# Performance work log

Hardware: AMD Instinct MI355X
Metric: run time of the kernel (lower is better)

The kernel has to match this reference:

```python
import jax, jax.numpy as jnp
from jax import lax
import numpy as np

K_NUM = 4
KD = KH = KW = 3
IN_CH = 32
OUT_CH = 64
ATT_HID = 8  # max(in_ch // max(4, min(8, in_ch//64)), 4) = max(32//4, 4)


def _build_freq_masks(kd, kh, kw, kernel_num):
    # Static (numpy) replica of build_3d_freq_masks: quantile-banded FFT energy masks.
    fd = np.fft.fftfreq(kd)
    fh = np.fft.fftfreq(kh)
    fw = np.fft.fftfreq(kw)
    FZ, FY, FX = np.meshgrid(fd, fh, fw, indexing='ij')
    energy = (FZ ** 2 + FY ** 2 + FX ** 2).ravel()
    bounds = np.quantile(energy, np.linspace(0.0, 1.0, kernel_num + 1), method='linear')
    masks = np.stack([(energy >= bounds[i]) & (energy <= bounds[i + 1]) for i in range(kernel_num)])
    return jnp.asarray(masks.reshape(kernel_num, kd, kh, kw), dtype=jnp.float32)


def setup_inputs() -> dict:
    key = jax.random.key(0)
    ks = jax.random.split(key, 7)
    x = jax.random.normal(ks[0], (2, IN_CH, 64, 64, 64), dtype=jnp.float32)
    freq_param = jax.random.normal(ks[1], (OUT_CH, IN_CH, KD, KH, KW, 2), dtype=jnp.float32) * 0.001
    att_w1 = jax.random.normal(ks[2], (ATT_HID, IN_CH), dtype=jnp.float32) * 0.1
    att_b1 = jnp.zeros((ATT_HID,), dtype=jnp.float32)
    att_w2 = jax.random.normal(ks[3], (K_NUM, ATT_HID), dtype=jnp.float32) * 0.1
    att_b2 = jnp.zeros((K_NUM,), dtype=jnp.float32)
    bias = jnp.zeros((OUT_CH,), dtype=jnp.float32)
    return {"x": x, "freq_param": freq_param, "att_w1": att_w1, "att_b1": att_b1,
            "att_w2": att_w2, "att_b2": att_b2, "bias": bias}


def reference(x, freq_param, att_w1, att_b1, att_w2, att_b2, bias):
    masks = _build_freq_masks(KD, KH, KW, K_NUM)  # (K, kd, kh, kw)
    # Frequency params -> complex -> banded -> spatial kernels via batched IFFT.
    freq = lax.complex(freq_param[..., 0], freq_param[..., 1])  # (O,I,kd,kh,kw) complex64
    masked = freq[None] * masks[:, None, None].astype(freq.dtype)  # (K,O,I,kd,kh,kw)
    kernels = jnp.fft.ifftn(masked, axes=(-3, -2, -1)).real.astype(x.dtype)
    # Per-sample attention over K experts: GAP -> 1x1 conv (linear) -> relu -> linear -> softmax.
    pooled = jnp.mean(x, axis=(2, 3, 4))  # (B, C)
    h = jax.nn.relu(pooled @ att_w1.T + att_b1)  # (B, hid)
    att = jax.nn.softmax(h @ att_w2.T + att_b2, axis=1)  # (B, K)
    out = jnp.zeros((x.shape[0], OUT_CH) + x.shape[2:], dtype=x.dtype)
    for k in range(K_NUM):  # fixed small expert count
        y_k = lax.conv_general_dilated(
            x, kernels[k], window_strides=(1, 1, 1),
            padding=[(1, 1)] * 3, rhs_dilation=(1, 1, 1),
            dimension_numbers=('NCDHW', 'OIDHW', 'NCDHW'))
        out = out + att[:, k][:, None, None, None, None] * y_k
    return out + bias[None, :, None, None, None]
```

## Files before the change

kernel.cpp:

```cpp
#include <hip/hip_runtime.h>

#define DIM 64
#define ICH 32
#define OCH 64
#define SPA (DIM*DIM*DIM)

typedef short  s16x8  __attribute__((ext_vector_type(8)));
typedef float  f32x16 __attribute__((ext_vector_type(16)));

__device__ __forceinline__ short f2bf(float f) {
    unsigned u = __float_as_uint(f);
    return (short)((u + 0x7fffu + ((u >> 16) & 1u)) >> 16);
}
__device__ __forceinline__ int swz(int a) { return a ^ (((a >> 7) & 7) << 4); }

__global__ __launch_bounds__(256) void pool_kernel(const float* __restrict__ x,
                                                   float* __restrict__ partial) {
    int bid = blockIdx.x;
    int pair = bid >> 5;
    int chunk = bid & 31;
    const float4* base = (const float4*)(x + (size_t)pair * SPA + (size_t)chunk * 8192);
    int tid = threadIdx.x;
    float s = 0.f;
#pragma unroll
    for (int k = 0; k < 8; ++k) {
        float4 v = base[k * 256 + tid];
        s += (v.x + v.y) + (v.z + v.w);
    }
#pragma unroll
    for (int off = 32; off > 0; off >>= 1) s += __shfl_down(s, off, 64);
    __shared__ float red[4];
    int lane = tid & 63, wv = tid >> 6;
    if (lane == 0) red[wv] = s;
    __syncthreads();
    if (tid == 0) partial[bid] = (red[0] + red[1]) + (red[2] + red[3]);
}

__global__ __launch_bounds__(64) void attn_kernel(const float* __restrict__ partial,
                                                  const float* __restrict__ w1,
                                                  const float* __restrict__ b1,
                                                  const float* __restrict__ w2,
                                                  const float* __restrict__ b2,
                                                  float* __restrict__ weff) {
    __shared__ float pl[64], hh[16], at[8];
    int t = threadIdx.x;
    {
        float s = 0.f;
#pragma unroll
        for (int k = 0; k < 32; ++k) s += partial[t * 32 + k];
        pl[t] = s * (1.0f / (float)SPA);
    }
    __syncthreads();
    if (t < 16) {
        int b = t >> 3, j = t & 7;
        float a = b1[j];
        for (int c = 0; c < 32; ++c) a += pl[b * 32 + c] * w1[j * 32 + c];
        hh[t] = a > 0.f ? a : 0.f;
    }
    __syncthreads();
    if (t < 8) {
        int b = t >> 2, k = t & 3;
        float a = b2[k];
        for (int j = 0; j < 8; ++j) a += hh[b * 8 + j] * w2[k * 8 + j];
        at[t] = a;
    }
    __syncthreads();
    if (t < 2) {
        float l0 = at[t*4], l1 = at[t*4+1], l2 = at[t*4+2], l3 = at[t*4+3];
        float m = fmaxf(fmaxf(l0, l1), fmaxf(l2, l3));
        float e0 = expf(l0 - m), e1 = expf(l1 - m), e2 = expf(l2 - m), e3 = expf(l3 - m);
        float inv = 1.0f / (e0 + e1 + e2 + e3);
        at[t*4] = e0 * inv; at[t*4+1] = e1 * inv; at[t*4+2] = e2 * inv; at[t*4+3] = e3 * inv;
    }
    __syncthreads();
    if (t < 54) {
        int b = t / 27, m = t % 27;
        int z = m / 9, y = (m / 3) % 3, xx = m % 3;
        int n = (z > 0) + (y > 0) + (xx > 0);
        float w = 0.f;
        w += at[b*4 + 0] * ((n <= 1) ? 1.f : 0.f);
        w += at[b*4 + 1] * ((n == 2) ? 1.f : 0.f);
        w += at[b*4 + 2] * ((n >= 2) ? 1.f : 0.f);
        w += at[b*4 + 3] * ((n == 3) ? 1.f : 0.f);
        weff[t] = w;
    }
}

__global__ __launch_bounds__(256) void ifft_kernel(const float* __restrict__ freq,
                                                   const float* __restrict__ weff,
                                                   short* __restrict__ keff) {
    int idx = blockIdx.x * 256 + threadIdx.x;
    int i = idx & 31;
    int o = (idx >> 5) & 63;
    int bt = idx >> 11;
    int t = bt % 27, b = bt / 27;
    int d = t / 9, h = (t / 3) % 3, w = t % 3;
    const float* f = freq + (size_t)(o * 32 + i) * 54;
    float s = 0.f;
#pragma unroll
    for (int z = 0; z < 3; ++z)
#pragma unroll
        for (int y = 0; y < 3; ++y)
#pragma unroll
            for (int xk = 0; xk < 3; ++xk) {
                int m = (d * z + h * y + w * xk) % 3;
                float cm = (m == 0) ? 1.0f : -0.5f;
                float sm = (m == 0) ? 0.0f : ((m == 1) ? 0.8660254037844386f
                                                       : -0.8660254037844386f);
                int tap = z * 9 + y * 3 + xk;
                s += weff[b * 27 + tap] * (f[tap * 2] * cm - f[tap * 2 + 1] * sm);
            }
    keff[idx] = f2bf(s * (1.0f / 27.0f));
}

__global__ __launch_bounds__(256, 2) void conv_mfma(const float* __restrict__ x,
                                                    const short* __restrict__ keff,
                                                    const float* __restrict__ bias,
                                                    float* __restrict__ out) {
    __shared__ char xs[34560];

    int bid = blockIdx.x;
    int wblk = bid & 3;
    int hblk = (bid >> 2) & 7;
    int dblk = (bid >> 5) & 15;
    int b    = bid >> 9;
    int d0 = dblk * 4, h0 = hblk * 8, w0 = wblk * 16;

    int tid = threadIdx.x;
    int l = tid & 63, td = tid >> 6;

    f32x16 acc[2][4];
#pragma unroll
    for (int i = 0; i < 2; ++i)
#pragma unroll
        for (int j = 0; j < 4; ++j) acc[i][j] = f32x16{};

    int laneB = td * 5760 + ((l >> 4) & 1) * 576 + (l & 15) * 32 + (l >> 5) * 16;
    const short* Abase = keff + (size_t)b * 55296 + (l & 31) * 32 + (l >> 5) * 8;
    int p0 = tid >> 1, half = tid & 1;

    for (int chunk = 0; chunk < 2; ++chunk) {
        __syncthreads();
        const float* xc = x + (size_t)(b * ICH + chunk * 16 + half * 8) * SPA;
#pragma unroll
        for (int it = 0; it < 9; ++it) {
            int e = it * 256 + tid;
            if (e < 2160) {
                int p = it * 128 + p0;
                int dd = p / 180, r = p - dd * 180;
                int hh2 = r / 18, ww2 = r - hh2 * 18;
                int gd = d0 - 1 + dd, gh = h0 - 1 + hh2, gw = w0 - 1 + ww2;
                s16x8 v = {};
                if ((unsigned)gd < 64u && (unsigned)gh < 64u && (unsigned)gw < 64u) {
                    const float* xp = xc + (((gd * 64) + gh) * 64 + gw);
#pragma unroll
                    for (int j = 0; j < 8; ++j) v[j] = f2bf(xp[(size_t)j * SPA]);
                }
                *(s16x8*)(xs + swz(e * 16)) = v;
            }
        }
        __syncthreads();

        const short* A = Abase + chunk * 16;
        s16x8 a0 = *(const s16x8*)(A);
        s16x8 a1 = *(const s16x8*)(A + 1024);
#pragma unroll 1
        for (int tap = 0; tap < 27; ++tap) {
            int nxt = (tap < 26) ? tap + 1 : 26;
            s16x8 n0 = *(const s16x8*)(A + nxt * 2048);
            s16x8 n1 = *(const s16x8*)(A + nxt * 2048 + 1024);
            int kd = tap / 9, rr = tap - kd * 9;
            int kh = rr / 3, kw2 = rr - kh * 3;
            int off = laneB + kd * 5760 + kh * 576 + kw2 * 32;
            s16x8 B0 = *(const s16x8*)(xs + swz(off));
            s16x8 B1 = *(const s16x8*)(xs + swz(off + 1152));
            s16x8 B2 = *(const s16x8*)(xs + swz(off + 2304));
            s16x8 B3 = *(const s16x8*)(xs + swz(off + 3456));
            acc[0][0] = __builtin_amdgcn_mfma_f32_32x32x16_bf16(a0, B0, acc[0][0], 0, 0, 0);
            acc[1][0] = __builtin_amdgcn_mfma_f32_32x32x16_bf16(a1, B0, acc[1][0], 0, 0, 0);
            acc[0][1] = __builtin_amdgcn_mfma_f32_32x32x16_bf16(a0, B1, acc[0][1], 0, 0, 0);
            acc[1][1] = __builtin_amdgcn_mfma_f32_32x32x16_bf16(a1, B1, acc[1][1], 0, 0, 0);
            acc[0][2] = __builtin_amdgcn_mfma_f32_32x32x16_bf16(a0, B2, acc[0][2], 0, 0, 0);
            acc[1][2] = __builtin_amdgcn_mfma_f32_32x32x16_bf16(a1, B2, acc[1][2], 0, 0, 0);
            acc[0][3] = __builtin_amdgcn_mfma_f32_32x32x16_bf16(a0, B3, acc[0][3], 0, 0, 0);
            acc[1][3] = __builtin_amdgcn_mfma_f32_32x32x16_bf16(a1, B3, acc[1][3], 0, 0, 0);
            a0 = n0; a1 = n1;
        }
    }

    float bv[32];
#pragma unroll
    for (int ot = 0; ot < 2; ++ot)
#pragma unroll
        for (int reg = 0; reg < 16; ++reg)
            bv[ot * 16 + reg] = bias[ot * 32 + (reg & 3) + 8 * (reg >> 2) + 4 * (l >> 5)];

    int dd = d0 + td;
    int ww2 = w0 + (l & 15);
    int hbase = h0 + ((l >> 4) & 1);
#pragma unroll
    for (int ot = 0; ot < 2; ++ot)
#pragma unroll
        for (int s = 0; s < 4; ++s) {
#pragma unroll
            for (int reg = 0; reg < 16; ++reg) {
                int o = ot * 32 + (reg & 3) + 8 * (reg >> 2) + 4 * (l >> 5);
                size_t oidx = (((size_t)(b * OCH + o) * DIM + dd) * DIM
                               + (hbase + 2 * s)) * DIM + ww2;
                out[oidx] = acc[ot][s][reg] + bv[ot * 16 + reg];
            }
        }
}

extern "C" void kernel_launch(void* const* d_in, const int* in_sizes, int n_in,
                              void* d_out, int out_size, void* d_ws, size_t ws_size,
                              hipStream_t stream) {
    const float* x    = (const float*)d_in[0];
    const float* freq = (const float*)d_in[1];
    const float* w1   = (const float*)d_in[2];
    const float* b1   = (const float*)d_in[3];
    const float* w2   = (const float*)d_in[4];
    const float* b2   = (const float*)d_in[5];
    const float* bias = (const float*)d_in[6];
    float* out = (float*)d_out;
    float* ws  = (float*)d_ws;

    float* partial = ws;
    float* weff    = ws + 2048;
    short* keff    = (short*)(ws + 2048 + 64);

    pool_kernel<<<2048, 256, 0, stream>>>(x, partial);
    attn_kernel<<<1, 64, 0, stream>>>(partial, w1, b1, w2, b2, weff);
    ifft_kernel<<<432, 256, 0, stream>>>(freq, weff, keff);
    conv_mfma<<<1024, 256, 0, stream>>>(x, keff, bias, out);
}
```

Baseline: 279.9 us.

## Pre-transpose input to channel-last bf16 and fuse pooling, attention and IFFT

Adds a prepass kernel that computes pooling partial sums and, in the same pass, writes x as a channel-last bf16 tensor. The conv kernel can then load 16-byte contiguous channel vectors instead of eight strided fp32 loads with per-element conversion. Attention and kernel synthesis are merged into one kernel, with each block redundantly recomputing the attention weights, which removes a launch. The cost is an extra 32MB bf16 write and read plus a dependence on workspace size, with the old path kept as a fallback.

```diff
diff --git a/kernel.cpp b/kernel.cpp
--- a/kernel.cpp
+++ b/kernel.cpp
@@ -12,49 +12,86 @@
     unsigned u = __float_as_uint(f);
     return (short)((u + 0x7fffu + ((u >> 16) & 1u)) >> 16);
 }
+__device__ __forceinline__ unsigned pk2bf(float lo, float hi) {
+    return (unsigned)(unsigned short)f2bf(lo) | ((unsigned)(unsigned short)f2bf(hi) << 16);
+}
 __device__ __forceinline__ int swz(int a) { return a ^ (((a >> 7) & 7) << 4); }
 
-__global__ __launch_bounds__(256) void pool_kernel(const float* __restrict__ x,
-                                                   float* __restrict__ partial) {
+
+__global__ __launch_bounds__(256) void prepass_kernel(const float* __restrict__ x,
+                                                      short* __restrict__ xT,
+                                                      float* __restrict__ partial) {
+    __shared__ unsigned lds32[64 * 17];
+    __shared__ float pacc[32];
+
     int bid = blockIdx.x;
-    int pair = bid >> 5;
-    int chunk = bid & 31;
-    const float4* base = (const float4*)(x + (size_t)pair * SPA + (size_t)chunk * 8192);
-    int tid = threadIdx.x;
-    float s = 0.f;
-#pragma unroll
-    for (int k = 0; k < 8; ++k) {
-        float4 v = base[k * 256 + tid];
-        s += (v.x + v.y) + (v.z + v.w);
-    }
-#pragma unroll
-    for (int off = 32; off > 0; off >>= 1) s += __shfl_down(s, off, 64);
-    __shared__ float red[4];
-    int lane = tid & 63, wv = tid >> 6;
-    if (lane == 0) red[wv] = s;
-    __syncthreads();
-    if (tid == 0) partial[bid] = (red[0] + red[1]) + (red[2] + red[3]);
-}
-
-__global__ __launch_bounds__(64) void attn_kernel(const float* __restrict__ partial,
-                                                  const float* __restrict__ w1,
-                                                  const float* __restrict__ b1,
-                                                  const float* __restrict__ w2,
-                                                  const float* __restrict__ b2,
-                                                  float* __restrict__ weff) {
-    __shared__ float pl[64], hh[16], at[8];
+    int hq = bid & 15, d = (bid >> 4) & 63, b = bid >> 10;
+    int t = threadIdx.x;
+    int cp = t >> 4;
+    int wg = t & 15;
+
+    float acc0 = 0.f, acc1 = 0.f;
+
+    for (int r = 0; r < 4; ++r) {
+        int h = hq * 4 + r;
+        const float* s0 = x + (size_t)(b * ICH + 2 * cp) * SPA + (d * 4096 + h * 64 + wg * 4);
+        float4 a = *(const float4*)s0;
+        float4 c = *(const float4*)(s0 + SPA);
+        acc0 += (a.x + a.y) + (a.z + a.w);
+        acc1 += (c.x + c.y) + (c.z + c.w);
+        __syncthreads();
+        lds32[(wg * 4 + 0) * 17 + cp] = pk2bf(a.x, c.x);
+        lds32[(wg * 4 + 1) * 17 + cp] = pk2bf(a.y, c.y);
+        lds32[(wg * 4 + 2) * 17 + cp] = pk2bf(a.z, c.z);
+        lds32[(wg * 4 + 3) * 17 + cp] = pk2bf(a.w, c.w);
+        __syncthreads();
+        int w = t >> 2, q = t & 3;
+        uint4 v;
+        v.x = lds32[w * 17 + q * 4 + 0];
+        v.y = lds32[w * 17 + q * 4 + 1];
+        v.z = lds32[w * 17 + q * 4 + 2];
+        v.w = lds32[w * 17 + q * 4 + 3];
+        *(uint4*)(xT + ((size_t)((b * 64 + d) * 64 + h) * 64 + w) * 32 + q * 8) = v;
+    }
+#pragma unroll
+    for (int off = 1; off < 16; off <<= 1) {
+        acc0 += __shfl_down(acc0, off, 64);
+        acc1 += __shfl_down(acc1, off, 64);
+    }
+    if (wg == 0) { pacc[2 * cp] = acc0; pacc[2 * cp + 1] = acc1; }
+    __syncthreads();
+    if (t < 32) partial[(size_t)(b * 32 + t) * 1024 + d * 16 + hq] = pacc[t];
+}
+
+__global__ __launch_bounds__(256) void attn_ifft_kernel(const float* __restrict__ partial,
+                                                        const float* __restrict__ freq,
+                                                        const float* __restrict__ w1,
+                                                        const float* __restrict__ b1,
+                                                        const float* __restrict__ w2,
+                                                        const float* __restrict__ b2,
+                                                        short* __restrict__ keff) {
+    __shared__ float red[256];
+    __shared__ float pooled[64];
+    __shared__ float hh[16], at[8], we[54];
     int t = threadIdx.x;
     {
+        int p = t >> 2, q = t & 3;
+        const float4* src = (const float4*)(partial + (size_t)p * 1024 + q * 256);
         float s = 0.f;
 #pragma unroll
-        for (int k = 0; k < 32; ++k) s += partial[t * 32 + k];
-        pl[t] = s * (1.0f / (float)SPA);
-    }
+        for (int k = 0; k < 64; ++k) {
+            float4 v = src[k];
+            s += (v.x + v.y) + (v.z + v.w);
+        }
+        red[t] = s;
+    }
+    __syncthreads();
+    if (t < 64) pooled[t] = (red[4*t] + red[4*t+1] + red[4*t+2] + red[4*t+3]) * (1.0f / (float)SPA);
     __syncthreads();
     if (t < 16) {
         int b = t >> 3, j = t & 7;
         float a = b1[j];
-        for (int c = 0; c < 32; ++c) a += pl[b * 32 + c] * w1[j * 32 + c];
+        for (int c = 0; c < 32; ++c) a += pooled[b * 32 + c] * w1[j * 32 + c];
         hh[t] = a > 0.f ? a : 0.f;
     }
     __syncthreads();
@@ -82,19 +119,15 @@
         w += at[b*4 + 1] * ((n == 2) ? 1.f : 0.f);
         w += at[b*4 + 2] * ((n >= 2) ? 1.f : 0.f);
         w += at[b*4 + 3] * ((n == 3) ? 1.f : 0.f);
-        weff[t] = w;
-    }
-}
-
-__global__ __launch_bounds__(256) void ifft_kernel(const float* __restrict__ freq,
-                                                   const float* __restrict__ weff,
-                                                   short* __restrict__ keff) {
-    int idx = blockIdx.x * 256 + threadIdx.x;
+        we[t] = w;
+    }
+    __syncthreads();
+    int idx = blockIdx.x * 256 + t;
     int i = idx & 31;
     int o = (idx >> 5) & 63;
     int bt = idx >> 11;
-    int t = bt % 27, b = bt / 27;
-    int d = t / 9, h = (t / 3) % 3, w = t % 3;
+    int tp = bt % 27, b = bt / 27;
+    int dk = tp / 9, hk = (tp / 3) % 3, wk = tp % 3;
     const float* f = freq + (size_t)(o * 32 + i) * 54;
     float s = 0.f;
 #pragma unroll
@@ -103,17 +136,17 @@
         for (int y = 0; y < 3; ++y)
 #pragma unroll
             for (int xk = 0; xk < 3; ++xk) {
-                int m = (d * z + h * y + w * xk) % 3;
+                int m = (dk * z + hk * y + wk * xk) % 3;
                 float cm = (m == 0) ? 1.0f : -0.5f;
                 float sm = (m == 0) ? 0.0f : ((m == 1) ? 0.8660254037844386f
                                                        : -0.8660254037844386f);
                 int tap = z * 9 + y * 3 + xk;
-                s += weff[b * 27 + tap] * (f[tap * 2] * cm - f[tap * 2 + 1] * sm);
+                s += we[b * 27 + tap] * (f[tap * 2] * cm - f[tap * 2 + 1] * sm);
             }
     keff[idx] = f2bf(s * (1.0f / 27.0f));
 }
 
-__global__ __launch_bounds__(256, 2) void conv_mfma(const float* __restrict__ x,
+__global__ __launch_bounds__(256, 2) void conv_fast(const short* __restrict__ xT,
                                                     const short* __restrict__ keff,
                                                     const float* __restrict__ bias,
                                                     float* __restrict__ out) {
@@ -137,25 +170,22 @@
 
     int laneB = td * 5760 + ((l >> 4) & 1) * 576 + (l & 15) * 32 + (l >> 5) * 16;
     const short* Abase = keff + (size_t)b * 55296 + (l & 31) * 32 + (l >> 5) * 8;
-    int p0 = tid >> 1, half = tid & 1;
+    const short* xTb = xT + (size_t)b * 8388608;
 
     for (int chunk = 0; chunk < 2; ++chunk) {
         __syncthreads();
-        const float* xc = x + (size_t)(b * ICH + chunk * 16 + half * 8) * SPA;
-#pragma unroll
-        for (int it = 0; it < 9; ++it) {
+        const short* xc = xTb + chunk * 16;
+#pragma unroll
+        for (int it = 0; it < 17; ++it) {
             int e = it * 256 + tid;
-            if (e < 2160) {
-                int p = it * 128 + p0;
+            if (e < 4320) {
+                int p = e >> 1, hf = e & 1;
                 int dd = p / 180, r = p - dd * 180;
                 int hh2 = r / 18, ww2 = r - hh2 * 18;
                 int gd = d0 - 1 + dd, gh = h0 - 1 + hh2, gw = w0 - 1 + ww2;
                 s16x8 v = {};
-                if ((unsigned)gd < 64u && (unsigned)gh < 64u && (unsigned)gw < 64u) {
-                    const float* xp = xc + (((gd * 64) + gh) * 64 + gw);
-#pragma unroll
-                    for (int j = 0; j < 8; ++j) v[j] = f2bf(xp[(size_t)j * SPA]);
-                }
+                if ((unsigned)gd < 64u && (unsigned)gh < 64u && (unsigned)gw < 64u)
+                    v = *(const s16x8*)(xc + ((gd * 64 + gh) * 64 + gw) * 32 + hf * 8);
                 *(s16x8*)(xs + swz(e * 16)) = v;
             }
         }
@@ -212,6 +242,197 @@
         }
 }
 
+
+__global__ __launch_bounds__(256) void pool_kernel(const float* __restrict__ x,
+                                                   float* __restrict__ partial) {
+    int bid = blockIdx.x;
+    int pair = bid >> 5;
+    int chunk = bid & 31;
+    const float4* base = (const float4*)(x + (size_t)pair * SPA + (size_t)chunk * 8192);
+    int tid = threadIdx.x;
+    float s = 0.f;
+#pragma unroll
+    for (int k = 0; k < 8; ++k) {
+        float4 v = base[k * 256 + tid];
+        s += (v.x + v.y) + (v.z + v.w);
+    }
+#pragma unroll
+    for (int off = 32; off > 0; off >>= 1) s += __shfl_down(s, off, 64);
+    __shared__ float red[4];
+    int lane = tid & 63, wv = tid >> 6;
+    if (lane == 0) red[wv] = s;
+    __syncthreads();
+    if (tid == 0) partial[bid] = (red[0] + red[1]) + (red[2] + red[3]);
+}
+
+__global__ __launch_bounds__(64) void attn_kernel(const float* __restrict__ partial,
+                                                  const float* __restrict__ w1,
+                                                  const float* __restrict__ b1,
+                                                  const float* __restrict__ w2,
+                                                  const float* __restrict__ b2,
+                                                  float* __restrict__ weff) {
+    __shared__ float pl[64], hh[16], at[8];
+    int t = threadIdx.x;
+    {
+        float s = 0.f;
+#pragma unroll
+        for (int k = 0; k < 32; ++k) s += partial[t * 32 + k];
+        pl[t] = s * (1.0f / (float)SPA);
+    }
+    __syncthreads();
+    if (t < 16) {
+        int b = t >> 3, j = t & 7;
+        float a = b1[j];
+        for (int c = 0; c < 32; ++c) a += pl[b * 32 + c] * w1[j * 32 + c];
+        hh[t] = a > 0.f ? a : 0.f;
+    }
+    __syncthreads();
+    if (t < 8) {
+        int b = t >> 2, k = t & 3;
+        float a = b2[k];
+        for (int j = 0; j < 8; ++j) a += hh[b * 8 + j] * w2[k * 8 + j];
+        at[t] = a;
+    }
+    __syncthreads();
+    if (t < 2) {
+        float l0 = at[t*4], l1 = at[t*4+1], l2 = at[t*4+2], l3 = at[t*4+3];
+        float m = fmaxf(fmaxf(l0, l1), fmaxf(l2, l3));
+        float e0 = expf(l0 - m), e1 = expf(l1 - m), e2 = expf(l2 - m), e3 = expf(l3 - m);
+        float inv = 1.0f / (e0 + e1 + e2 + e3);
+        at[t*4] = e0 * inv; at[t*4+1] = e1 * inv; at[t*4+2] = e2 * inv; at[t*4+3] = e3 * inv;
+    }
+    __syncthreads();
+    if (t < 54) {
+        int b = t / 27, m = t % 27;
+        int z = m / 9, y = (m / 3) % 3, xx = m % 3;
+        int n = (z > 0) + (y > 0) + (xx > 0);
+        float w = 0.f;
+        w += at[b*4 + 0] * ((n <= 1) ? 1.f : 0.f);
+        w += at[b*4 + 1] * ((n == 2) ? 1.f : 0.f);
+        w += at[b*4 + 2] * ((n >= 2) ? 1.f : 0.f);
+        w += at[b*4 + 3] * ((n == 3) ? 1.f : 0.f);
+        weff[t] = w;
+    }
+}
+
+__global__ __launch_bounds__(256) void ifft_kernel(const float* __restrict__ freq,
+                                                   const float* __restrict__ weff,
+                                                   short* __restrict__ keff) {
+    int idx = blockIdx.x * 256 + threadIdx.x;
+    int i = idx & 31;
+    int o = (idx >> 5) & 63;
+    int bt = idx >> 11;
+    int t = bt % 27, b = bt / 27;
+    int d = t / 9, h = (t / 3) % 3, w = t % 3;
+    const float* f = freq + (size_t)(o * 32 + i) * 54;
+    float s = 0.f;
+#pragma unroll
+    for (int z = 0; z < 3; ++z)
+#pragma unroll
+        for (int y = 0; y < 3; ++y)
+#pragma unroll
+            for (int xk = 0; xk < 3; ++xk) {
+                int m = (d * z + h * y + w * xk) % 3;
+                float cm = (m == 0) ? 1.0f : -0.5f;
+                float sm = (m == 0) ? 0.0f : ((m == 1) ? 0.8660254037844386f
+                                                       : -0.8660254037844386f);
+                int tap = z * 9 + y * 3 + xk;
+                s += weff[b * 27 + tap] * (f[tap * 2] * cm - f[tap * 2 + 1] * sm);
+            }
+    keff[idx] = f2bf(s * (1.0f / 27.0f));
+}
+
+__global__ __launch_bounds__(256, 2) void conv_mfma(const float* __restrict__ x,
+                                                    const short* __restrict__ keff,
+                                                    const float* __restrict__ bias,
+                                                    float* __restrict__ out) {
+    __shared__ char xs[34560];
+    int bid = blockIdx.x;
+    int wblk = bid & 3;
+    int hblk = (bid >> 2) & 7;
+    int dblk = (bid >> 5) & 15;
+    int b    = bid >> 9;
+    int d0 = dblk * 4, h0 = hblk * 8, w0 = wblk * 16;
+    int tid = threadIdx.x;
+    int l = tid & 63, td = tid >> 6;
+    f32x16 acc[2][4];
+#pragma unroll
+    for (int i = 0; i < 2; ++i)
+#pragma unroll
+        for (int j = 0; j < 4; ++j) acc[i][j] = f32x16{};
+    int laneB = td * 5760 + ((l >> 4) & 1) * 576 + (l & 15) * 32 + (l >> 5) * 16;
+    const short* Abase = keff + (size_t)b * 55296 + (l & 31) * 32 + (l >> 5) * 8;
+    int p0 = tid >> 1, half = tid & 1;
+    for (int chunk = 0; chunk < 2; ++chunk) {
+        __syncthreads();
+        const float* xc = x + (size_t)(b * ICH + chunk * 16 + half * 8) * SPA;
+#pragma unroll
+        for (int it = 0; it < 9; ++it) {
+            int e = it * 256 + tid;
+            if (e < 2160) {
+                int p = it * 128 + p0;
+                int dd = p / 180, r = p - dd * 180;
+                int hh2 = r / 18, ww2 = r - hh2 * 18;
+                int gd = d0 - 1 + dd, gh = h0 - 1 + hh2, gw = w0 - 1 + ww2;
+                s16x8 v = {};
+                if ((unsigned)gd < 64u && (unsigned)gh < 64u && (unsigned)gw < 64u) {
+                    const float* xp = xc + (((gd * 64) + gh) * 64 + gw);
+#pragma unroll
+                    for (int j = 0; j < 8; ++j) v[j] = f2bf(xp[(size_t)j * SPA]);
+                }
+                *(s16x8*)(xs + swz(e * 16)) = v;
+            }
+        }
+        __syncthreads();
+        const short* A = Abase + chunk * 16;
+        s16x8 a0 = *(const s16x8*)(A);
+        s16x8 a1 = *(const s16x8*)(A + 1024);
+#pragma unroll 1
+        for (int tap = 0; tap < 27; ++tap) {
+            int nxt = (tap < 26) ? tap + 1 : 26;
+            s16x8 n0 = *(const s16x8*)(A + nxt * 2048);
+            s16x8 n1 = *(const s16x8*)(A + nxt * 2048 + 1024);
+            int kd = tap / 9, rr = tap - kd * 9;
+            int kh = rr / 3, kw2 = rr - kh * 3;
+            int off = laneB + kd * 5760 + kh * 576 + kw2 * 32;
+            s16x8 B0 = *(const s16x8*)(xs + swz(off));
+            s16x8 B1 = *(const s16x8*)(xs + swz(off + 1152));
+            s16x8 B2 = *(const s16x8*)(xs + swz(off + 2304));
+            s16x8 B3 = *(const s16x8*)(xs + swz(off + 3456));
+            acc[0][0] = __builtin_amdgcn_mfma_f32_32x32x16_bf16(a0, B0, acc[0][0], 0, 0, 0);
+            acc[1][0] = __builtin_amdgcn_mfma_f32_32x32x16_bf16(a1, B0, acc[1][0], 0, 0, 0);
+            acc[0][1] = __builtin_amdgcn_mfma_f32_32x32x16_bf16(a0, B1, acc[0][1], 0, 0, 0);
+            acc[1][1] = __builtin_amdgcn_mfma_f32_32x32x16_bf16(a1, B1, acc[1][1], 0, 0, 0);
+            acc[0][2] = __builtin_amdgcn_mfma_f32_32x32x16_bf16(a0, B2, acc[0][2], 0, 0, 0);
+            acc[1][2] = __builtin_amdgcn_mfma_f32_32x32x16_bf16(a1, B2, acc[1][2], 0, 0, 0);
+            acc[0][3] = __builtin_amdgcn_mfma_f32_32x32x16_bf16(a0, B3, acc[0][3], 0, 0, 0);
+            acc[1][3] = __builtin_amdgcn_mfma_f32_32x32x16_bf16(a1, B3, acc[1][3], 0, 0, 0);
+            a0 = n0; a1 = n1;
+        }
+    }
+    float bv[32];
+#pragma unroll
+    for (int ot = 0; ot < 2; ++ot)
+#pragma unroll
+        for (int reg = 0; reg < 16; ++reg)
+            bv[ot * 16 + reg] = bias[ot * 32 + (reg & 3) + 8 * (reg >> 2) + 4 * (l >> 5)];
+    int dd = d0 + td;
+    int ww2 = w0 + (l & 15);
+    int hbase = h0 + ((l >> 4) & 1);
+#pragma unroll
+    for (int ot = 0; ot < 2; ++ot)
+#pragma unroll
+        for (int s = 0; s < 4; ++s) {
+#pragma unroll
+            for (int reg = 0; reg < 16; ++reg) {
+                int o = ot * 32 + (reg & 3) + 8 * (reg >> 2) + 4 * (l >> 5);
+                size_t oidx = (((size_t)(b * OCH + o) * DIM + dd) * DIM
+                               + (hbase + 2 * s)) * DIM + ww2;
+                out[oidx] = acc[ot][s][reg] + bv[ot * 16 + reg];
+            }
+        }
+}
+
 extern "C" void kernel_launch(void* const* d_in, const int* in_sizes, int n_in,
                               void* d_out, int out_size, void* d_ws, size_t ws_size,
                               hipStream_t stream) {
@@ -223,14 +444,25 @@
     const float* b2   = (const float*)d_in[5];
     const float* bias = (const float*)d_in[6];
     float* out = (float*)d_out;
-    float* ws  = (float*)d_ws;
-
-    float* partial = ws;
-    float* weff    = ws + 2048;
-    short* keff    = (short*)(ws + 2048 + 64);
-
-    pool_kernel<<<2048, 256, 0, stream>>>(x, partial);
-    attn_kernel<<<1, 64, 0, stream>>>(partial, w1, b1, w2, b2, weff);
-    ifft_kernel<<<432, 256, 0, stream>>>(freq, weff, keff);
-    conv_mfma<<<1024, 256, 0, stream>>>(x, keff, bias, out);
-}
+    char* ws = (char*)d_ws;
+
+    const size_t NEED = 524288 + (size_t)2 * 64 * 64 * 64 * 32 * 2;
+    if (ws_size >= NEED) {
+        float* partial = (float*)ws;
+        short* keff    = (short*)(ws + 262144);
+        short* xT      = (short*)(ws + 524288);
+
+        prepass_kernel<<<2048, 256, 0, stream>>>(x, xT, partial);
+        attn_ifft_kernel<<<432, 256, 0, stream>>>(partial, freq, w1, b1, w2, b2, keff);
+        conv_fast<<<1024, 256, 0, stream>>>(xT, keff, bias, out);
+    } else {
+        float* partial = (float*)ws;
+        float* weff    = (float*)(ws + 8192);
+        short* keff    = (short*)(ws + 8448);
+
+        pool_kernel<<<2048, 256, 0, stream>>>(x, partial);
+        attn_kernel<<<1, 64, 0, stream>>>(partial, w1, b1, w2, b2, weff);
+        ifft_kernel<<<432, 256, 0, stream>>>(freq, weff, keff);
+        conv_mfma<<<1024, 256, 0, stream>>>(x, keff, bias, out);
+    }
+}
```

Measured after the change: 307.6 us. 1.1x slower.
